# Optimization experiments

Measured on AMD Instinct MI355X. Metric: run time of the kernel, lower is better.

## Reference

```python
import jax, jax.numpy as jnp
import numpy as np

D_MODEL = 1024
NUM_HEADS = 16
HEAD_DIM = D_MODEL // NUM_HEADS
B, S = 2, 2048


def setup_inputs() -> dict:
    key = jax.random.key(0)
    ks = jax.random.split(key, 5)
    x = jax.random.normal(ks[0], (B, S, D_MODEL), dtype=jnp.float32)
    # nn.Linear weights are [out_features, in_features]
    Wq = jax.random.normal(ks[1], (D_MODEL, D_MODEL), dtype=jnp.float32) / np.sqrt(D_MODEL)
    Wk = jax.random.normal(ks[2], (HEAD_DIM, D_MODEL), dtype=jnp.float32) / np.sqrt(D_MODEL)
    Wv = jax.random.normal(ks[3], (HEAD_DIM, D_MODEL), dtype=jnp.float32) / np.sqrt(D_MODEL)
    Wo = jax.random.normal(ks[4], (D_MODEL, D_MODEL), dtype=jnp.float32) / np.sqrt(D_MODEL)
    # causal mask, broadcastable to [B, H, S, S]; mask==0 positions get -inf
    mask = jnp.tril(jnp.ones((S, S), dtype=bool))[None, None]
    return {"x": x, "Wq": Wq, "Wk": Wk, "Wv": Wv, "Wo": Wo, "mask": mask}


def reference(x, Wq, Wk, Wv, Wo, mask):
    Bsz, Sl, D = x.shape
    H, hd = NUM_HEADS, HEAD_DIM
    q = (x @ Wq.T).reshape(Bsz, Sl, H, hd)          # [B,S,H,hd]
    k = x @ Wk.T                                    # [B,S,hd] (single shared KV head)
    v = x @ Wv.T                                    # [B,S,hd]
    scale = 1.0 / np.sqrt(hd).astype(np.float32)
    # scores: [B,H,S,S] — full O(n^2) matrix, as in the original module
    scores = jnp.einsum('bshd,btd->bhst', q, k) * scale
    scores = jnp.where(mask, scores, -jnp.inf)
    attn = jax.nn.softmax(scores, axis=-1)
    out = jnp.einsum('bhst,btd->bshd', attn, v).reshape(Bsz, Sl, D)
    return out @ Wo.T
```

## Files before the change

### kernel.cpp

```cpp
#include <hip/hip_runtime.h>
#include <hip/hip_bf16.h>
#include <math.h>

#define BB 2
#define SS 2048
#define DD 1024
#define NH 16
#define HD 64
#define MM (BB * SS)

typedef __hip_bfloat16 bf16;
typedef __bf16 bf16_t;
typedef __attribute__((ext_vector_type(8))) __bf16 bf16x8;
typedef __attribute__((ext_vector_type(4))) __bf16 bf16x4;
typedef __attribute__((ext_vector_type(4))) float floatx4;

#define SCALEQ 0.18033688011112042f

__global__ void detect_dtype(const unsigned int* __restrict__ x, int* __restrict__ flag) {
    const int tid = threadIdx.x;
    int good = 0;
    for (int i = tid; i < 256; i += 64) {
        unsigned int bits = (x[i] & 0xFFFFu) << 16;
        float v = __uint_as_float(bits);
        float av = fabsf(v);
        if (av == 0.f || (av >= 9.5367431640625e-7f && av <= 64.f)) good++;
    }
#pragma unroll
    for (int s = 1; s < 64; s <<= 1) good += __shfl_xor(good, s);
    if (tid == 0) *flag = (good >= 240) ? 0 : 1;
}

#define BK 32
#define KP 40

__device__ __forceinline__ bf16x4 cvt4(float4 v) {
    bf16x4 o;
    o[0] = (bf16_t)v.x; o[1] = (bf16_t)v.y; o[2] = (bf16_t)v.z; o[3] = (bf16_t)v.w;
    return o;
}

__global__ __launch_bounds__(256) void proj_qkv(const void* __restrict__ X,
                                                const void* __restrict__ Wq,
                                                const void* __restrict__ Wk,
                                                const void* __restrict__ Wv,
                                                bf16_t* __restrict__ QA,
                                                bf16_t* __restrict__ Kp,
                                                bf16_t* __restrict__ VpT,
                                                const int* __restrict__ flag) {
    const int f = *flag;

    __shared__ bf16_t As[128 * KP];
    __shared__ bf16_t Ws[64 * KP];

    const int tid = threadIdx.x;
    const int wave = tid >> 6, lane = tid & 63;
    const int lo = lane & 15, quad = lane >> 4;
    const int rb = wave * 32;
    const int cb = blockIdx.x;
    const int rowBase = blockIdx.y * 128;

    floatx4 acc[2][4];
#pragma unroll
    for (int i = 0; i < 2; i++)
#pragma unroll
        for (int j = 0; j < 4; j++) acc[i][j] = (floatx4){0.f, 0.f, 0.f, 0.f};

    if (f) {
        const int rA = tid >> 3, sg = tid & 7;
        const float* arow[4];
        const float* wrow[2];
#pragma unroll
        for (int p = 0; p < 4; p++)
            arow[p] = (const float*)X + (size_t)(rowBase + rA + 32 * p) * DD;
#pragma unroll
        for (int p = 0; p < 2; p++) {
            int row = rA + 32 * p;
            if (cb < 16)       wrow[p] = (const float*)Wq + (size_t)(cb * 64 + row) * DD;
            else if (cb == 16) wrow[p] = (const float*)Wk + (size_t)row * DD;
            else               wrow[p] = (const float*)Wv + (size_t)row * DD;
        }
        float4 aR[4], wR[2];
#pragma unroll
        for (int p = 0; p < 4; p++) aR[p] = *(const float4*)(arow[p] + sg * 4);
#pragma unroll
        for (int p = 0; p < 2; p++) wR[p] = *(const float4*)(wrow[p] + sg * 4);

        for (int k0 = 0; k0 < DD; k0 += BK) {
            __syncthreads();
#pragma unroll
            for (int p = 0; p < 4; p++)
                *(bf16x4*)&As[(rA + 32 * p) * KP + sg * 4] = cvt4(aR[p]);
#pragma unroll
            for (int p = 0; p < 2; p++)
                *(bf16x4*)&Ws[(rA + 32 * p) * KP + sg * 4] = cvt4(wR[p]);
            __syncthreads();
            if (k0 + BK < DD) {
#pragma unroll
                for (int p = 0; p < 4; p++) aR[p] = *(const float4*)(arow[p] + k0 + BK + sg * 4);
#pragma unroll
                for (int p = 0; p < 2; p++) wR[p] = *(const float4*)(wrow[p] + k0 + BK + sg * 4);
            }
            bf16x8 afr[2], bfr[4];
#pragma unroll
            for (int i = 0; i < 2; i++)
                afr[i] = *(const bf16x8*)&As[(rb + i * 16 + lo) * KP + quad * 8];
#pragma unroll
            for (int j = 0; j < 4; j++)
                bfr[j] = *(const bf16x8*)&Ws[(j * 16 + lo) * KP + quad * 8];
#pragma unroll
            for (int i = 0; i < 2; i++)
#pragma unroll
                for (int j = 0; j < 4; j++)
                    acc[i][j] = __builtin_amdgcn_mfma_f32_16x16x32_bf16(afr[i], bfr[j], acc[i][j], 0, 0, 0);
        }
    } else {
        const int rA = tid >> 2, sg = tid & 3;
        const bf16_t* arow[2];
        const bf16_t* wrow;
#pragma unroll
        for (int p = 0; p < 2; p++)
            arow[p] = (const bf16_t*)X + (size_t)(rowBase + rA + 64 * p) * DD;
        if (cb < 16)       wrow = (const bf16_t*)Wq + (size_t)(cb * 64 + rA) * DD;
        else if (cb == 16) wrow = (const bf16_t*)Wk + (size_t)rA * DD;
        else               wrow = (const bf16_t*)Wv + (size_t)rA * DD;
        bf16x8 aR[2], wR;
#pragma unroll
        for (int p = 0; p < 2; p++) aR[p] = *(const bf16x8*)(arow[p] + sg * 8);
        wR = *(const bf16x8*)(wrow + sg * 8);

        for (int k0 = 0; k0 < DD; k0 += BK) {
            __syncthreads();
#pragma unroll
            for (int p = 0; p < 2; p++)
                *(bf16x8*)&As[(rA + 64 * p) * KP + sg * 8] = aR[p];
            *(bf16x8*)&Ws[rA * KP + sg * 8] = wR;
            __syncthreads();
            if (k0 + BK < DD) {
#pragma unroll
                for (int p = 0; p < 2; p++) aR[p] = *(const bf16x8*)(arow[p] + k0 + BK + sg * 8);
                wR = *(const bf16x8*)(wrow + k0 + BK + sg * 8);
            }
            bf16x8 afr[2], bfr[4];
#pragma unroll
            for (int i = 0; i < 2; i++)
                afr[i] = *(const bf16x8*)&As[(rb + i * 16 + lo) * KP + quad * 8];
#pragma unroll
            for (int j = 0; j < 4; j++)
                bfr[j] = *(const bf16x8*)&Ws[(j * 16 + lo) * KP + quad * 8];
#pragma unroll
            for (int i = 0; i < 2; i++)
#pragma unroll
                for (int j = 0; j < 4; j++)
                    acc[i][j] = __builtin_amdgcn_mfma_f32_16x16x32_bf16(afr[i], bfr[j], acc[i][j], 0, 0, 0);
        }
    }

#pragma unroll
    for (int i = 0; i < 2; i++)
#pragma unroll
        for (int j = 0; j < 4; j++)
#pragma unroll
            for (int reg = 0; reg < 4; reg++) {
                int row = rowBase + rb + i * 16 + quad * 4 + reg;
                int col = j * 16 + lo;
                if (cb < 16) {
                    QA[(size_t)row * DD + cb * 64 + col] = (bf16_t)(acc[i][j][reg] * SCALEQ);
                } else if (cb == 16) {
                    Kp[(size_t)row * HD + col] = (bf16_t)acc[i][j][reg];
                } else {
                    VpT[((size_t)(row >> 11) * HD + col) * SS + (row & (SS - 1))] =
                        (bf16_t)acc[i][j][reg];
                }
            }
}

__global__ __launch_bounds__(256) void proj_o(const bf16_t* __restrict__ AO,
                                              const void* __restrict__ Wo,
                                              void* __restrict__ Cout,
                                              const int* __restrict__ flag) {
    const int f = *flag;

    __shared__ bf16_t As[128 * KP];
    __shared__ bf16_t Ws[64 * KP];

    const int tid = threadIdx.x;
    const int wave = tid >> 6, lane = tid & 63;
    const int lo = lane & 15, quad = lane >> 4;
    const int rb = wave * 32;
    const int colBase = blockIdx.x * 64;
    const int rowBase = blockIdx.y * 128;

    floatx4 acc[2][4];
#pragma unroll
    for (int i = 0; i < 2; i++)
#pragma unroll
        for (int j = 0; j < 4; j++) acc[i][j] = (floatx4){0.f, 0.f, 0.f, 0.f};

    const int rA2 = tid >> 2, sgA = tid & 3;
    const bf16_t* arow[2] = {AO + (size_t)(rowBase + rA2) * DD,
                             AO + (size_t)(rowBase + rA2 + 64) * DD};
    bf16x8 aR[2];
#pragma unroll
    for (int p = 0; p < 2; p++) aR[p] = *(const bf16x8*)(arow[p] + sgA * 8);

    if (f) {
        const int rW = tid >> 3, sgW = tid & 7;
        const float* wrow[2];
#pragma unroll
        for (int p = 0; p < 2; p++)
            wrow[p] = (const float*)Wo + (size_t)(colBase + rW + 32 * p) * DD;
        float4 wR[2];
#pragma unroll
        for (int p = 0; p < 2; p++) wR[p] = *(const float4*)(wrow[p] + sgW * 4);

        for (int k0 = 0; k0 < DD; k0 += BK) {
            __syncthreads();
#pragma unroll
            for (int p = 0; p < 2; p++)
                *(bf16x8*)&As[(rA2 + 64 * p) * KP + sgA * 8] = aR[p];
#pragma unroll
            for (int p = 0; p < 2; p++)
                *(bf16x4*)&Ws[(rW + 32 * p) * KP + sgW * 4] = cvt4(wR[p]);
            __syncthreads();
            if (k0 + BK < DD) {
#pragma unroll
                for (int p = 0; p < 2; p++) aR[p] = *(const bf16x8*)(arow[p] + k0 + BK + sgA * 8);
#pragma unroll
                for (int p = 0; p < 2; p++) wR[p] = *(const float4*)(wrow[p] + k0 + BK + sgW * 4);
            }
            bf16x8 afr[2], bfr[4];
#pragma unroll
            for (int i = 0; i < 2; i++)
                afr[i] = *(const bf16x8*)&As[(rb + i * 16 + lo) * KP + quad * 8];
#pragma unroll
            for (int j = 0; j < 4; j++)
                bfr[j] = *(const bf16x8*)&Ws[(j * 16 + lo) * KP + quad * 8];
#pragma unroll
            for (int i = 0; i < 2; i++)
#pragma unroll
                for (int j = 0; j < 4; j++)
                    acc[i][j] = __builtin_amdgcn_mfma_f32_16x16x32_bf16(afr[i], bfr[j], acc[i][j], 0, 0, 0);
        }
    } else {
        const bf16_t* wrow = (const bf16_t*)Wo + (size_t)(colBase + rA2) * DD;
        bf16x8 wR = *(const bf16x8*)(wrow + sgA * 8);

        for (int k0 = 0; k0 < DD; k0 += BK) {
            __syncthreads();
#pragma unroll
            for (int p = 0; p < 2; p++)
                *(bf16x8*)&As[(rA2 + 64 * p) * KP + sgA * 8] = aR[p];
            *(bf16x8*)&Ws[rA2 * KP + sgA * 8] = wR;
            __syncthreads();
            if (k0 + BK < DD) {
#pragma unroll
                for (int p = 0; p < 2; p++) aR[p] = *(const bf16x8*)(arow[p] + k0 + BK + sgA * 8);
                wR = *(const bf16x8*)(wrow + k0 + BK + sgA * 8);
            }
            bf16x8 afr[2], bfr[4];
#pragma unroll
            for (int i = 0; i < 2; i++)
                afr[i] = *(const bf16x8*)&As[(rb + i * 16 + lo) * KP + quad * 8];
#pragma unroll
            for (int j = 0; j < 4; j++)
                bfr[j] = *(const bf16x8*)&Ws[(j * 16 + lo) * KP + quad * 8];
#pragma unroll
            for (int i = 0; i < 2; i++)
#pragma unroll
                for (int j = 0; j < 4; j++)
                    acc[i][j] = __builtin_amdgcn_mfma_f32_16x16x32_bf16(afr[i], bfr[j], acc[i][j], 0, 0, 0);
        }
    }

#pragma unroll
    for (int i = 0; i < 2; i++)
#pragma unroll
        for (int j = 0; j < 4; j++)
#pragma unroll
            for (int reg = 0; reg < 4; reg++) {
                int row = rowBase + rb + i * 16 + quad * 4 + reg;
                int col = colBase + j * 16 + lo;
                size_t idx = (size_t)row * DD + col;
                if (f) ((float*)Cout)[idx] = acc[i][j][reg];
                else   ((bf16_t*)Cout)[idx] = (bf16_t)acc[i][j][reg];
            }
}

#define PSTR 40
#define DMTHR 8.0f

__global__ __launch_bounds__(512, 4) void attn_mfma(const bf16_t* Q,
                                                    const bf16_t* __restrict__ K,
                                                    const bf16_t* __restrict__ Vt,
                                                    bf16_t* O) {
    const int h = blockIdx.y, b = blockIdx.z;
    const int tid = threadIdx.x;
    const int wq = tid >> 6, lane = tid & 63;
    const int lo = lane & 15, quad = lane >> 4;
    const int x = blockIdx.x;

    const int nA = x + 1;
    int na = 1, bestc = 0x7fffffff;
#pragma unroll
    for (int a = 1; a <= 7; ++a) {
        int cA = (nA + a - 1) / a;
        int cB = (65 - nA + (7 - a)) / (8 - a);
        int c = cA > cB ? cA : cB;
        if (c < bestc) { bestc = c; na = a; }
    }
    int qt, pos, gs;
    if (wq < na) { qt = x;      pos = wq;      gs = na; }
    else         { qt = 63 - x; pos = wq - na; gs = 8 - na; }
    const int q0 = qt * 32;
    const int n = qt + 1;
    const int itS = (n * pos) / gs;
    const int itE = (n * (pos + 1)) / gs;

    __shared__ __align__(16) char smem[4 * 32 * 64 * 4];
    __shared__ float MrgML[4][2][2][16];
    bf16_t* Pw = (bf16_t*)smem + wq * (32 * PSTR);
    float (*MrgO)[32 * 64] = (float (*)[32 * 64])smem;

    bf16x8 qf[2][2];
#pragma unroll
    for (int s = 0; s < 2; s++)
#pragma unroll
        for (int hf = 0; hf < 2; hf++)
            qf[s][hf] = *(const bf16x8*)(Q + ((size_t)(b * SS + q0 + s * 16 + lo)) * DD +
                                         h * HD + hf * 32 + quad * 8);

    floatx4 Oacc[2][4];
    float m_i[2], l_ln[2];
#pragma unroll
    for (int s = 0; s < 2; s++) {
#pragma unroll
        for (int dt = 0; dt < 4; dt++) Oacc[s][dt] = (floatx4){0.f, 0.f, 0.f, 0.f};
        m_i[s] = -1e30f; l_ln[s] = 0.f;
    }

    const bf16_t* Kb = K + (size_t)b * SS * HD;
    const bf16_t* Vb = Vt + (size_t)b * HD * SS;

    if (itS < itE) {
        bf16x8 kf[2][2];
#pragma unroll
        for (int kt = 0; kt < 2; kt++)
#pragma unroll
            for (int hf = 0; hf < 2; hf++)
                kf[kt][hf] = *(const bf16x8*)(Kb + (size_t)(itS * 32 + kt * 16 + lo) * HD +
                                              hf * 32 + quad * 8);

        for (int it = itS; it < itE; it++) {
            const int t0 = it * 32;

            bf16x8 vf[4];
#pragma unroll
            for (int dt = 0; dt < 4; dt++)
                vf[dt] = *(const bf16x8*)(Vb + (size_t)(dt * 16 + lo) * SS + t0 + quad * 8);

            bf16x8 kn[2][2];
            if (it + 1 < itE) {
#pragma unroll
                for (int kt = 0; kt < 2; kt++)
#pragma unroll
                    for (int hf = 0; hf < 2; hf++)
                        kn[kt][hf] = *(const bf16x8*)(Kb + (size_t)(t0 + 32 + kt * 16 + lo) * HD +
                                                      hf * 32 + quad * 8);
            }

            floatx4 st[2][2];
#pragma unroll
            for (int s = 0; s < 2; s++)
#pragma unroll
                for (int kt = 0; kt < 2; kt++) {
                    floatx4 z = (floatx4){0.f, 0.f, 0.f, 0.f};
                    z = __builtin_amdgcn_mfma_f32_16x16x32_bf16(kf[kt][0], qf[s][0], z, 0, 0, 0);
                    z = __builtin_amdgcn_mfma_f32_16x16x32_bf16(kf[kt][1], qf[s][1], z, 0, 0, 0);
                    st[s][kt] = z;
                }

            if (it == qt) {
#pragma unroll
                for (int s = 0; s < 2; s++) {
                    int q = q0 + s * 16 + lo;
#pragma unroll
                    for (int kt = 0; kt < 2; kt++)
#pragma unroll
                        for (int reg = 0; reg < 4; reg++)
                            if (t0 + kt * 16 + quad * 4 + reg > q) st[s][kt][reg] = -1e30f;
                }
            }

#pragma unroll
            for (int s = 0; s < 2; s++) {
                float lm = fmaxf(fmaxf(fmaxf(st[s][0][0], st[s][0][1]), fmaxf(st[s][0][2], st[s][0][3])),
                                 fmaxf(fmaxf(st[s][1][0], st[s][1][1]), fmaxf(st[s][1][2], st[s][1][3])));
                if (__any(lm > m_i[s] + DMTHR)) {
                    float mx = fmaxf(lm, __shfl_xor(lm, 16));
                    mx = fmaxf(mx, __shfl_xor(mx, 32));
                    float mn = fmaxf(m_i[s], mx);
                    float al = exp2f(m_i[s] - mn);
                    m_i[s] = mn;
                    l_ln[s] *= al;
#pragma unroll
                    for (int dt = 0; dt < 4; dt++) Oacc[s][dt] *= al;
                }
                float p[2][4];
#pragma unroll
                for (int kt = 0; kt < 2; kt++)
#pragma unroll
                    for (int reg = 0; reg < 4; reg++)
                        p[kt][reg] = exp2f(st[s][kt][reg] - m_i[s]);
                l_ln[s] += ((p[0][0] + p[0][1]) + (p[0][2] + p[0][3])) +
                           ((p[1][0] + p[1][1]) + (p[1][2] + p[1][3]));
#pragma unroll
                for (int kt = 0; kt < 2; kt++) {
                    bf16x4 pk;
#pragma unroll
                    for (int reg = 0; reg < 4; reg++) pk[reg] = (bf16_t)p[kt][reg];
                    *(bf16x4*)&Pw[(s * 16 + lo) * PSTR + kt * 16 + quad * 4] = pk;
                }
            }

            asm volatile("s_waitcnt lgkmcnt(0)" ::: "memory");

            bf16x8 pb[2];
#pragma unroll
            for (int s = 0; s < 2; s++)
                pb[s] = *(const bf16x8*)&Pw[(s * 16 + lo) * PSTR + quad * 8];
#pragma unroll
            for (int s = 0; s < 2; s++)
#pragma unroll
                for (int dt = 0; dt < 4; dt++)
                    Oacc[s][dt] = __builtin_amdgcn_mfma_f32_16x16x32_bf16(vf[dt], pb[s], Oacc[s][dt], 0, 0, 0);

#pragma unroll
            for (int kt = 0; kt < 2; kt++)
#pragma unroll
                for (int hf = 0; hf < 2; hf++) kf[kt][hf] = kn[kt][hf];
        }
    }

    float l_i[2];
#pragma unroll
    for (int s = 0; s < 2; s++) {
        float l = l_ln[s];
        l += __shfl_xor(l, 16);
        l += __shfl_xor(l, 32);
        l_i[s] = l;
    }

    for (int step = 1; step < 8; step <<= 1) {
        const bool pub = (pos & (2 * step - 1)) == step;
        const bool cmb = ((pos & (2 * step - 1)) == 0) && (pos + step < gs);
        __syncthreads();
        if (pub) {
            float* Ob = MrgO[wq >> 1];
#pragma unroll
            for (int s = 0; s < 2; s++) {
#pragma unroll
                for (int dt = 0; dt < 4; dt++)
#pragma unroll
                    for (int reg = 0; reg < 4; reg++)
                        Ob[(s * 16 + dt * 4 + reg) * 64 + lane] = Oacc[s][dt][reg];
                if (quad == 0) {
                    MrgML[wq >> 1][s][0][lo] = m_i[s];
                    MrgML[wq >> 1][s][1][lo] = l_i[s];
                }
            }
        }
        __syncthreads();
        if (cmb) {
            const int bu = (wq + step) >> 1;
            const float* Ob = MrgO[bu];
#pragma unroll
            for (int s = 0; s < 2; s++) {
                float m1 = MrgML[bu][s][0][lo];
                float l1 = MrgML[bu][s][1][lo];
                float mm = fmaxf(m_i[s], m1);
                float a0 = exp2f(m_i[s] - mm);
                float a1 = exp2f(m1 - mm);
                m_i[s] = mm;
                l_i[s] = l_i[s] * a0 + l1 * a1;
#pragma unroll
                for (int dt = 0; dt < 4; dt++)
#pragma unroll
                    for (int reg = 0; reg < 4; reg++)
                        Oacc[s][dt][reg] = Oacc[s][dt][reg] * a0 +
                                           Ob[(s * 16 + dt * 4 + reg) * 64 + lane] * a1;
            }
        }
    }

    if (pos == 0) {
#pragma unroll
        for (int s = 0; s < 2; s++) {
            float linv = 1.f / l_i[s];
            bf16_t* Orow = O + ((size_t)(b * SS + q0 + s * 16 + lo)) * DD + h * HD;
#pragma unroll
            for (int dt = 0; dt < 4; dt++) {
                bf16x4 ov;
#pragma unroll
                for (int reg = 0; reg < 4; reg++)
                    ov[reg] = (bf16_t)(Oacc[s][dt][reg] * linv);
                *(bf16x4*)&Orow[dt * 16 + quad * 4] = ov;
            }
        }
    }
}

extern "C" void kernel_launch(void* const* d_in, const int* in_sizes, int n_in,
                              void* d_out, int out_size, void* d_ws, size_t ws_size,
                              hipStream_t stream) {
    const void* x  = d_in[0];
    const void* Wq = d_in[1];
    const void* Wk = d_in[2];
    const void* Wv = d_in[3];
    const void* Wo = d_in[4];

    char* ws = (char*)d_ws;
    int* flag = (int*)ws;
    bf16_t* QA  = (bf16_t*)(ws + 256);
    bf16_t* Kp  = QA + (size_t)MM * DD;
    bf16_t* VpT = Kp + (size_t)MM * HD;

    detect_dtype<<<1, 64, 0, stream>>>((const unsigned int*)x, flag);

    proj_qkv<<<dim3(18, MM / 128), dim3(256), 0, stream>>>(x, Wq, Wk, Wv, QA, Kp, VpT, flag);

    attn_mfma<<<dim3(32, NH, BB), dim3(512), 0, stream>>>(QA, Kp, VpT, QA);

    proj_o<<<dim3(16, MM / 128), dim3(256), 0, stream>>>(QA, Wo, d_out, flag);
}
```

Baseline: 219.0 us.

## Pre-convert inputs to bf16, drop K prefetch, raise attention occupancy

Adds a conv_all kernel that converts x and all weights to bf16 in workspace up front, so the projection GEMMs read bf16 instead of converting fp32 on the fly. The attention loop no longer prefetches the next K tile, and the rescale check covers both rows in one __any. Launch bounds rise from 4 to 6 waves-per-EU to reduce register pressure. The conversion pass adds an extra full read and write of the inputs and another kernel launch, and removing the prefetch may expose K load latency.

```diff
diff --git a/kernel.cpp b/kernel.cpp
--- a/kernel.cpp
+++ b/kernel.cpp
@@ -28,7 +28,48 @@
     }
 #pragma unroll
     for (int s = 1; s < 64; s <<= 1) good += __shfl_xor(good, s);
-    if (tid == 0) *flag = (good >= 240) ? 0 : 1;
+    if (tid == 0) { flag[0] = (good >= 240) ? 0 : 1; flag[1] = 0; }
+}
+
+__device__ __forceinline__ void conv_seg(const void* __restrict__ in,
+                                         bf16_t* __restrict__ out,
+                                         int n, int f, int tid, int T) {
+    if (f) {
+        const float* p = (const float*)in;
+        for (int i = tid * 8; i < n; i += T * 8) {
+            float4 a = *(const float4*)(p + i);
+            float4 b = *(const float4*)(p + i + 4);
+            bf16x8 o;
+            o[0] = (bf16_t)a.x; o[1] = (bf16_t)a.y; o[2] = (bf16_t)a.z; o[3] = (bf16_t)a.w;
+            o[4] = (bf16_t)b.x; o[5] = (bf16_t)b.y; o[6] = (bf16_t)b.z; o[7] = (bf16_t)b.w;
+            *(bf16x8*)(out + i) = o;
+        }
+    } else {
+        const bf16_t* p = (const bf16_t*)in;
+        for (int i = tid * 8; i < n; i += T * 8)
+            *(bf16x8*)(out + i) = *(const bf16x8*)(p + i);
+    }
+}
+
+__global__ __launch_bounds__(256) void conv_all(const void* __restrict__ x,
+                                                const void* __restrict__ wq,
+                                                const void* __restrict__ wk,
+                                                const void* __restrict__ wv,
+                                                const void* __restrict__ wo,
+                                                bf16_t* __restrict__ xb,
+                                                bf16_t* __restrict__ wqb,
+                                                bf16_t* __restrict__ wkb,
+                                                bf16_t* __restrict__ wvb,
+                                                bf16_t* __restrict__ wob,
+                                                const int* __restrict__ flag) {
+    const int f = *flag;
+    const int tid = blockIdx.x * blockDim.x + threadIdx.x;
+    const int T = gridDim.x * blockDim.x;
+    conv_seg(x, xb, MM * DD, f, tid, T);
+    conv_seg(wq, wqb, DD * DD, f, tid, T);
+    conv_seg(wk, wkb, HD * DD, f, tid, T);
+    conv_seg(wv, wvb, HD * DD, f, tid, T);
+    conv_seg(wo, wob, DD * DD, f, tid, T);
 }
 
 #define BK 32
@@ -178,8 +219,10 @@
 __global__ __launch_bounds__(256) void proj_o(const bf16_t* __restrict__ AO,
                                               const void* __restrict__ Wo,
                                               void* __restrict__ Cout,
-                                              const int* __restrict__ flag) {
-    const int f = *flag;
+                                              const int* __restrict__ flagW,
+                                              const int* __restrict__ flagOut) {
+    const int f = *flagW;
+    const int fout = *flagOut;
 
     __shared__ bf16_t As[128 * KP];
     __shared__ bf16_t Ws[64 * KP];
@@ -282,15 +325,15 @@
                 int row = rowBase + rb + i * 16 + quad * 4 + reg;
                 int col = colBase + j * 16 + lo;
                 size_t idx = (size_t)row * DD + col;
-                if (f) ((float*)Cout)[idx] = acc[i][j][reg];
-                else   ((bf16_t*)Cout)[idx] = (bf16_t)acc[i][j][reg];
+                if (fout) ((float*)Cout)[idx] = acc[i][j][reg];
+                else      ((bf16_t*)Cout)[idx] = (bf16_t)acc[i][j][reg];
             }
 }
 
 #define PSTR 40
 #define DMTHR 8.0f
 
-__global__ __launch_bounds__(512, 4) void attn_mfma(const bf16_t* Q,
+__global__ __launch_bounds__(512, 6) void attn_mfma(const bf16_t* Q,
                                                     const bf16_t* __restrict__ K,
                                                     const bf16_t* __restrict__ Vt,
                                                     bf16_t* O) {
@@ -342,104 +385,96 @@
     const bf16_t* Kb = K + (size_t)b * SS * HD;
     const bf16_t* Vb = Vt + (size_t)b * HD * SS;
 
-    if (itS < itE) {
+    for (int it = itS; it < itE; it++) {
+        const int t0 = it * 32;
+
         bf16x8 kf[2][2];
 #pragma unroll
         for (int kt = 0; kt < 2; kt++)
 #pragma unroll
             for (int hf = 0; hf < 2; hf++)
-                kf[kt][hf] = *(const bf16x8*)(Kb + (size_t)(itS * 32 + kt * 16 + lo) * HD +
+                kf[kt][hf] = *(const bf16x8*)(Kb + (size_t)(t0 + kt * 16 + lo) * HD +
                                               hf * 32 + quad * 8);
 
-        for (int it = itS; it < itE; it++) {
-            const int t0 = it * 32;
-
-            bf16x8 vf[4];
+        floatx4 st[2][2];
+#pragma unroll
+        for (int s = 0; s < 2; s++)
+#pragma unroll
+            for (int kt = 0; kt < 2; kt++) {
+                floatx4 z = (floatx4){0.f, 0.f, 0.f, 0.f};
+                z = __builtin_amdgcn_mfma_f32_16x16x32_bf16(kf[kt][0], qf[s][0], z, 0, 0, 0);
+                z = __builtin_amdgcn_mfma_f32_16x16x32_bf16(kf[kt][1], qf[s][1], z, 0, 0, 0);
+                st[s][kt] = z;
+            }
+
+        if (it == qt) {
+#pragma unroll
+            for (int s = 0; s < 2; s++) {
+                int q = q0 + s * 16 + lo;
+#pragma unroll
+                for (int kt = 0; kt < 2; kt++)
+#pragma unroll
+                    for (int reg = 0; reg < 4; reg++)
+                        if (t0 + kt * 16 + quad * 4 + reg > q) st[s][kt][reg] = -1e30f;
+            }
+        }
+
+        float lm[2];
+#pragma unroll
+        for (int s = 0; s < 2; s++)
+            lm[s] = fmaxf(fmaxf(fmaxf(st[s][0][0], st[s][0][1]), fmaxf(st[s][0][2], st[s][0][3])),
+                          fmaxf(fmaxf(st[s][1][0], st[s][1][1]), fmaxf(st[s][1][2], st[s][1][3])));
+        if (__any((lm[0] > m_i[0] + DMTHR) || (lm[1] > m_i[1] + DMTHR))) {
+#pragma unroll
+            for (int s = 0; s < 2; s++) {
+                float mx = fmaxf(lm[s], __shfl_xor(lm[s], 16));
+                mx = fmaxf(mx, __shfl_xor(mx, 32));
+                float mn = fmaxf(m_i[s], mx);
+                float al = exp2f(m_i[s] - mn);
+                m_i[s] = mn;
+                l_ln[s] *= al;
+#pragma unroll
+                for (int dt = 0; dt < 4; dt++) Oacc[s][dt] *= al;
+            }
+        }
+
+#pragma unroll
+        for (int s = 0; s < 2; s++) {
+#pragma unroll
+            for (int kt = 0; kt < 2; kt++)
+#pragma unroll
+                for (int reg = 0; reg < 4; reg++)
+                    st[s][kt][reg] = exp2f(st[s][kt][reg] - m_i[s]);
+            l_ln[s] += ((st[s][0][0] + st[s][0][1]) + (st[s][0][2] + st[s][0][3])) +
+                       ((st[s][1][0] + st[s][1][1]) + (st[s][1][2] + st[s][1][3]));
+        }
+
+#pragma unroll
+        for (int s = 0; s < 2; s++)
+#pragma unroll
+            for (int kt = 0; kt < 2; kt++) {
+                bf16x4 pk;
+#pragma unroll
+                for (int reg = 0; reg < 4; reg++) pk[reg] = (bf16_t)st[s][kt][reg];
+                *(bf16x4*)&Pw[(s * 16 + lo) * PSTR + kt * 16 + quad * 4] = pk;
+            }
+
+        bf16x8 vf[4];
+#pragma unroll
+        for (int dt = 0; dt < 4; dt++)
+            vf[dt] = *(const bf16x8*)(Vb + (size_t)(dt * 16 + lo) * SS + t0 + quad * 8);
+
+        asm volatile("s_waitcnt lgkmcnt(0)" ::: "memory");
+
+        bf16x8 pb[2];
+#pragma unroll
+        for (int s = 0; s < 2; s++)
+            pb[s] = *(const bf16x8*)&Pw[(s * 16 + lo) * PSTR + quad * 8];
+#pragma unroll
+        for (int s = 0; s < 2; s++)
 #pragma unroll
             for (int dt = 0; dt < 4; dt++)
-                vf[dt] = *(const bf16x8*)(Vb + (size_t)(dt * 16 + lo) * SS + t0 + quad * 8);
-
-            bf16x8 kn[2][2];
-            if (it + 1 < itE) {
-#pragma unroll
-                for (int kt = 0; kt < 2; kt++)
-#pragma unroll
-                    for (int hf = 0; hf < 2; hf++)
-                        kn[kt][hf] = *(const bf16x8*)(Kb + (size_t)(t0 + 32 + kt * 16 + lo) * HD +
-                                                      hf * 32 + quad * 8);
-            }
-
-            floatx4 st[2][2];
-#pragma unroll
-            for (int s = 0; s < 2; s++)
-#pragma unroll
-                for (int kt = 0; kt < 2; kt++) {
-                    floatx4 z = (floatx4){0.f, 0.f, 0.f, 0.f};
-                    z = __builtin_amdgcn_mfma_f32_16x16x32_bf16(kf[kt][0], qf[s][0], z, 0, 0, 0);
-                    z = __builtin_amdgcn_mfma_f32_16x16x32_bf16(kf[kt][1], qf[s][1], z, 0, 0, 0);
-                    st[s][kt] = z;
-                }
-
-            if (it == qt) {
-#pragma unroll
-                for (int s = 0; s < 2; s++) {
-                    int q = q0 + s * 16 + lo;
-#pragma unroll
-                    for (int kt = 0; kt < 2; kt++)
-#pragma unroll
-                        for (int reg = 0; reg < 4; reg++)
-                            if (t0 + kt * 16 + quad * 4 + reg > q) st[s][kt][reg] = -1e30f;
-                }
-            }
-
-#pragma unroll
-            for (int s = 0; s < 2; s++) {
-                float lm = fmaxf(fmaxf(fmaxf(st[s][0][0], st[s][0][1]), fmaxf(st[s][0][2], st[s][0][3])),
-                                 fmaxf(fmaxf(st[s][1][0], st[s][1][1]), fmaxf(st[s][1][2], st[s][1][3])));
-                if (__any(lm > m_i[s] + DMTHR)) {
-                    float mx = fmaxf(lm, __shfl_xor(lm, 16));
-                    mx = fmaxf(mx, __shfl_xor(mx, 32));
-                    float mn = fmaxf(m_i[s], mx);
-                    float al = exp2f(m_i[s] - mn);
-                    m_i[s] = mn;
-                    l_ln[s] *= al;
-#pragma unroll
-                    for (int dt = 0; dt < 4; dt++) Oacc[s][dt] *= al;
-                }
-                float p[2][4];
-#pragma unroll
-                for (int kt = 0; kt < 2; kt++)
-#pragma unroll
-                    for (int reg = 0; reg < 4; reg++)
-                        p[kt][reg] = exp2f(st[s][kt][reg] - m_i[s]);
-                l_ln[s] += ((p[0][0] + p[0][1]) + (p[0][2] + p[0][3])) +
-                           ((p[1][0] + p[1][1]) + (p[1][2] + p[1][3]));
-#pragma unroll
-                for (int kt = 0; kt < 2; kt++) {
-                    bf16x4 pk;
-#pragma unroll
-                    for (int reg = 0; reg < 4; reg++) pk[reg] = (bf16_t)p[kt][reg];
-                    *(bf16x4*)&Pw[(s * 16 + lo) * PSTR + kt * 16 + quad * 4] = pk;
-                }
-            }
-
-            asm volatile("s_waitcnt lgkmcnt(0)" ::: "memory");
-
-            bf16x8 pb[2];
-#pragma unroll
-            for (int s = 0; s < 2; s++)
-                pb[s] = *(const bf16x8*)&Pw[(s * 16 + lo) * PSTR + quad * 8];
-#pragma unroll
-            for (int s = 0; s < 2; s++)
-#pragma unroll
-                for (int dt = 0; dt < 4; dt++)
-                    Oacc[s][dt] = __builtin_amdgcn_mfma_f32_16x16x32_bf16(vf[dt], pb[s], Oacc[s][dt], 0, 0, 0);
-
-#pragma unroll
-            for (int kt = 0; kt < 2; kt++)
-#pragma unroll
-                for (int hf = 0; hf < 2; hf++) kf[kt][hf] = kn[kt][hf];
-        }
+                Oacc[s][dt] = __builtin_amdgcn_mfma_f32_16x16x32_bf16(vf[dt], pb[s], Oacc[s][dt], 0, 0, 0);
     }
 
     float l_i[2];
@@ -524,12 +559,28 @@
     bf16_t* QA  = (bf16_t*)(ws + 256);
     bf16_t* Kp  = QA + (size_t)MM * DD;
     bf16_t* VpT = Kp + (size_t)MM * HD;
+    bf16_t* Xb  = VpT + (size_t)BB * HD * SS;
+    bf16_t* Wqb = Xb + (size_t)MM * DD;
+    bf16_t* Wkb = Wqb + (size_t)DD * DD;
+    bf16_t* Wvb = Wkb + (size_t)HD * DD;
+    bf16_t* Wob = Wvb + (size_t)HD * DD;
+    size_t need = (size_t)((char*)(Wob + (size_t)DD * DD) - ws);
 
     detect_dtype<<<1, 64, 0, stream>>>((const unsigned int*)x, flag);
 
-    proj_qkv<<<dim3(18, MM / 128), dim3(256), 0, stream>>>(x, Wq, Wk, Wv, QA, Kp, VpT, flag);
-
-    attn_mfma<<<dim3(32, NH, BB), dim3(512), 0, stream>>>(QA, Kp, VpT, QA);
-
-    proj_o<<<dim3(16, MM / 128), dim3(256), 0, stream>>>(QA, Wo, d_out, flag);
-}
+    if (ws_size >= need) {
+        conv_all<<<dim3(1024), dim3(256), 0, stream>>>(x, Wq, Wk, Wv, Wo,
+                                                       Xb, Wqb, Wkb, Wvb, Wob, flag);
+        proj_qkv<<<dim3(18, MM / 128), dim3(256), 0, stream>>>(Xb, Wqb, Wkb, Wvb,
+                                                               QA, Kp, VpT, flag + 1);
+        attn_mfma<<<dim3(32, NH, BB), dim3(512), 0, stream>>>(QA, Kp, VpT, QA);
+        proj_o<<<dim3(16, MM / 128), dim3(256), 0, stream>>>(QA, Wob, d_out,
+                                                             flag + 1, flag);
+    } else {
+        proj_qkv<<<dim3(18, MM / 128), dim3(256), 0, stream>>>(x, Wq, Wk, Wv,
+                                                               QA, Kp, VpT, flag);
+        attn_mfma<<<dim3(32, NH, BB), dim3(512), 0, stream>>>(QA, Kp, VpT, QA);
+        proj_o<<<dim3(16, MM / 128), dim3(256), 0, stream>>>(QA, Wo, d_out,
+                                                             flag, flag);
+    }
+}
```

Result: slower. 283.0 us (+29.2%).
